# Kernel optimization log

Measured on AMD Instinct MI355X. Metric: run time of the kernel, lower is better.

The kernel has to match this reference:

```python
import jax, jax.numpy as jnp
import numpy as np

N_ENT = 100000
N_REL = 500
D_IN = 128
D_OUT = 128
E_HALF = 1000000  # edges per direction; edge_index has 2*E_HALF columns
BN_EPS = 1e-5


def ccorr(a, b):
    # circular correlation: irfft(conj(rfft(a)) * rfft(b))
    d = a.shape[-1]
    return jnp.fft.irfft(jnp.conj(jnp.fft.rfft(a, axis=-1)) * jnp.fft.rfft(b, axis=-1), n=d, axis=-1)


def setup_inputs() -> dict:
    key = jax.random.key(0)
    ks = jax.random.split(key, 12)
    inv = 1.0 / np.sqrt(D_IN)
    inp = {
        "x": jax.random.normal(ks[0], (N_ENT, D_IN), dtype=jnp.float32),
        "rel_embed": jax.random.normal(ks[1], (N_REL, D_IN), dtype=jnp.float32),
        "w_in": jax.random.uniform(ks[2], (D_IN, D_OUT), minval=-inv, maxval=inv, dtype=jnp.float32),
        "w_out": jax.random.uniform(ks[3], (D_IN, D_OUT), minval=-inv, maxval=inv, dtype=jnp.float32),
        "w_loop": jax.random.uniform(ks[4], (D_IN, D_OUT), minval=-inv, maxval=inv, dtype=jnp.float32),
        "w_rel": jax.random.uniform(ks[5], (D_IN, D_OUT), minval=-inv, maxval=inv, dtype=jnp.float32),
        "loop_rel": jax.random.normal(ks[6], (1, D_IN), dtype=jnp.float32),
        "bias": jnp.zeros((D_OUT,), dtype=jnp.float32),
        "bn_weight": jnp.ones((D_OUT,), dtype=jnp.float32),
        "bn_bias": jnp.zeros((D_OUT,), dtype=jnp.float32),
        "edge_index": jax.random.randint(ks[7], (2, 2 * E_HALF), 0, N_ENT, dtype=jnp.int32),
        "edge_type": jax.random.randint(ks[8], (2 * E_HALF,), 0, N_REL, dtype=jnp.int32),
    }
    return inp


def _compute_norm(edge_index, num_ent):
    row, col = edge_index[0], edge_index[1]
    ones = jnp.ones(row.shape, dtype=jnp.float32)
    deg = jax.ops.segment_sum(ones, row, num_segments=num_ent)
    deg_inv = jnp.where(deg > 0, jax.lax.rsqrt(jnp.maximum(deg, 1.0)), 0.0)
    return deg_inv[row] * deg_inv[col]  # [E]


def _propagate(x, edge_index, edge_type, rel_all, weight, norm, num_ent):
    x_j = x[edge_index[0]]              # [E, d_in] gather source nodes
    r = rel_all[edge_type]              # [E, d_in] gather relation embeds
    m = ccorr(x_j, r) @ weight          # [E, d_out]
    if norm is not None:
        m = m * norm[:, None]
    return jax.ops.segment_sum(m, edge_index[1], num_segments=num_ent)


def reference(x, rel_embed, w_in, w_out, w_loop, w_rel, loop_rel, bias, bn_weight, bn_bias, edge_index, edge_type):
    num_ent = x.shape[0]
    rel_all = jnp.concatenate([rel_embed, loop_rel], axis=0)  # [R+1, d_in]
    e = edge_index.shape[1] // 2
    in_idx, out_idx = edge_index[:, :e], edge_index[:, e:]
    in_type, out_type = edge_type[:e], edge_type[e:]

    in_norm = _compute_norm(in_idx, num_ent)
    out_norm = _compute_norm(out_idx, num_ent)

    in_res = _propagate(x, in_idx, in_type, rel_all, w_in, in_norm, num_ent)
    out_res = _propagate(x, out_idx, out_type, rel_all, w_out, out_norm, num_ent)
    # loop edges are (i, i) with relation = last row of rel_all -> identity scatter
    loop_res = ccorr(x, rel_all[-1][None, :]) @ w_loop

    out = (in_res + out_res + loop_res) * (1.0 / 3.0) + bias
    # BatchNorm1d (training-mode batch statistics, biased variance)
    mu = jnp.mean(out, axis=0)
    var = jnp.mean((out - mu) ** 2, axis=0)
    out = (out - mu) * jax.lax.rsqrt(var + BN_EPS) * bn_weight + bn_bias

    rel_out = (rel_all @ w_rel)[:-1]
    return out, rel_out
```

## Files before the change

kernel.cpp:

```cpp
#include <hip/hip_runtime.h>
#include <cmath>

#define N_ENT 100000
#define EHALF 1000000
#define N_REL 500
#define NBUK 196
#define DPB 512
#define SCAP 7680
#define DCAP 6656
#define NSB 512
#define SPAN 1954
#define XFB 391

#ifndef M_PI
#define M_PI 3.14159265358979323846
#endif

typedef _Float16 f16x8 __attribute__((ext_vector_type(8)));
typedef _Float16 f16x4 __attribute__((ext_vector_type(4)));
typedef _Float16 f16x2 __attribute__((ext_vector_type(2)));
typedef float f32x4 __attribute__((ext_vector_type(4)));

union H16 { unsigned short u; _Float16 h; };
union HU32 { unsigned u; f16x2 h; };

__global__ void k_tabs(float* __restrict__ Ftab, float* __restrict__ Gtab,
                       _Float16* __restrict__ FtabT,
                       int* __restrict__ gcur, float* __restrict__ bnAcc) {
  if (blockIdx.x == 0) {
    for (int j = threadIdx.x; j < 4 * NBUK; j += 256) gcur[j] = 0;
    bnAcc[threadIdx.x] = 0.f;
  }
  int i = blockIdx.x * 256 + threadIdx.x;
  if (i >= 128 * 128) return;
  int n = i >> 7, s = i & 127;
  float fv, gv;
  if (s == 0) { fv = 1.f; gv = 1.f / 384.f; }
  else if (s == 1) { float sg = (n & 1) ? -1.f : 1.f; fv = sg; gv = sg / 384.f; }
  else {
    int f = s >> 1;
    double ang = 2.0 * M_PI * (double)((f * n) & 127) / 128.0;
    if (!(s & 1)) { double c = cos(ang); fv = (float)c; gv = (float)(c * (2.0 / 384.0)); }
    else { double sv = sin(ang); fv = (float)(-sv); gv = (float)(-sv * (2.0 / 384.0)); }
  }
  Ftab[n * 128 + s] = fv;
  Gtab[s * 128 + n] = gv;
  FtabT[s * 128 + n] = (_Float16)fv;
}

__device__ void gemm128_body(char* smem, const float* __restrict__ A, int lda,
                             const float* __restrict__ B,
                             float* __restrict__ C, int ldc,
                             int M, int K, int m0) {
  float (*As)[64] = (float(*)[64])smem;
  float (*Bs)[128] = (float(*)[128])(smem + 64 * 64 * 4);
  const int t = threadIdx.x;
  const int cg = t & 31;
  const int eg = t >> 5;
  float acc[8][4];
#pragma unroll
  for (int i = 0; i < 8; ++i)
#pragma unroll
    for (int j = 0; j < 4; ++j) acc[i][j] = 0.f;

  for (int k0 = 0; k0 < K; k0 += 64) {
#pragma unroll
    for (int p = 0; p < 4; ++p) {
      int idx = t + p * 256;
      int r = idx >> 4, c4 = idx & 15;
      int gr = m0 + r;
      float4 v = make_float4(0.f, 0.f, 0.f, 0.f);
      if (gr < M) v = *(const float4*)(A + (size_t)gr * lda + k0 + c4 * 4);
      *(float4*)&As[r][c4 * 4] = v;
    }
#pragma unroll
    for (int p = 0; p < 8; ++p) {
      int idx = t + p * 256;
      int r = idx >> 5, c4 = idx & 31;
      float4 v = *(const float4*)(B + (size_t)(k0 + r) * 128 + c4 * 4);
      *(float4*)&Bs[r][c4 * 4] = v;
    }
    __syncthreads();
#pragma unroll
    for (int k = 0; k < 64; ++k) {
      float4 bv = *(float4*)&Bs[k][cg * 4];
#pragma unroll
      for (int i = 0; i < 8; ++i) {
        float av = As[eg * 8 + i][k];
        acc[i][0] += av * bv.x; acc[i][1] += av * bv.y;
        acc[i][2] += av * bv.z; acc[i][3] += av * bv.w;
      }
    }
    __syncthreads();
  }
#pragma unroll
  for (int i = 0; i < 8; ++i) {
    int gr = m0 + eg * 8 + i;
    if (gr < M) {
      float4 v = make_float4(acc[i][0], acc[i][1], acc[i][2], acc[i][3]);
      *(float4*)(C + (size_t)gr * ldc + cg * 4) = v;
    }
  }
}

__device__ inline f16x8 loadAfrag(const _Float16* A, size_t off) {
  return *(const f16x8*)(A + off);
}
__device__ inline f16x8 loadAfrag(const float* A, size_t off) {
  float4 u = *(const float4*)(A + off);
  float4 v = *(const float4*)(A + off + 4);
  return (f16x8){(_Float16)u.x, (_Float16)u.y, (_Float16)u.z, (_Float16)u.w,
                 (_Float16)v.x, (_Float16)v.y, (_Float16)v.z, (_Float16)v.w};
}

template<int K, int KS, int MODE, typename AT>
__device__ void mgemm_body(char* lds, int bid,
                           const AT* __restrict__ A, int lda,
                           const _Float16* __restrict__ BT,
                           _Float16* __restrict__ C, int ldc, int M,
                           const float* __restrict__ bias, float* __restrict__ bnAcc) {
  const int t = threadIdx.x;
  const int l = t & 63, w = t >> 6;
  const int col0 = l & 15, rg = l >> 4;
  const int rowbase = bid * 256 + w * 64;
  const int sw = (col0 & 7) << 4;

  f32x4 acc[4][8];
  f32x4 zz = {0.f, 0.f, 0.f, 0.f};
#pragma unroll
  for (int a = 0; a < 4; ++a)
#pragma unroll
    for (int n = 0; n < 8; ++n) acc[a][n] = zz;

  for (int ks0 = 0; ks0 < K; ks0 += KS) {
    __syncthreads();
    const int CH = KS / 8;
    for (int u = t; u < 128 * CH; u += 256) {
      int col = u / CH, kc = u % CH;
      f16x8 vch = *(const f16x8*)(BT + (size_t)col * K + ks0 + kc * 8);
      *(f16x8*)(lds + col * (KS * 2) + ((kc * 16) ^ ((col & 7) << 4))) = vch;
    }
    __syncthreads();
#pragma unroll
    for (int ks = 0; ks < KS / 32; ++ks) {
      int kb = ks0 + ks * 32 + rg * 8;
      f16x8 af[4];
#pragma unroll
      for (int a = 0; a < 4; ++a) {
        int rb = rowbase + a * 16;
        if (rb < M) af[a] = loadAfrag(A, (size_t)(rb + col0) * lda + kb);
        else af[a] = (f16x8){0, 0, 0, 0, 0, 0, 0, 0};
      }
      int kc = ks * 4 + rg;
#pragma unroll
      for (int n = 0; n < 8; ++n) {
        f16x8 bf = *(const f16x8*)(lds + (n * 16 + col0) * (KS * 2) + ((kc * 16) ^ sw));
#pragma unroll
        for (int a = 0; a < 4; ++a)
          acc[a][n] = __builtin_amdgcn_mfma_f32_16x16x32_f16(af[a], bf, acc[a][n], 0, 0, 0);
      }
    }
  }

  if (MODE == 1) {
#pragma unroll
    for (int a = 0; a < 4; ++a) {
      int rb = rowbase + a * 16;
      if (rb >= M) continue;
#pragma unroll
      for (int r = 0; r < 4; ++r) {
        int row = rb + rg * 4 + r;
#pragma unroll
        for (int n = 0; n < 8; ++n) {
          int col = n * 16 + col0;
          C[(size_t)row * ldc + col] = (_Float16)acc[a][n][r];
        }
      }
    }
  } else {
    float sacc[8], qacc[8];
#pragma unroll
    for (int n = 0; n < 8; ++n) { sacc[n] = 0.f; qacc[n] = 0.f; }
#pragma unroll
    for (int a = 0; a < 4; ++a) {
      int rb = rowbase + a * 16;
      if (rb >= M) continue;
#pragma unroll
      for (int n = 0; n < 8; ++n) {
        int col = n * 16 + col0;
        float bi = bias[col];
#pragma unroll
        for (int r = 0; r < 4; ++r) {
          float val = acc[a][n][r] + bi;
          C[(size_t)(rb + rg * 4 + r) * ldc + col] = (_Float16)val;
          sacc[n] += val; qacc[n] += val * val;
        }
      }
    }
    __syncthreads();
    float* Sb = (float*)lds;
    float* Qb = Sb + 512;
#pragma unroll
    for (int n = 0; n < 8; ++n) {
      float s = sacc[n], q = qacc[n];
      s += __shfl_xor(s, 16); s += __shfl_xor(s, 32);
      q += __shfl_xor(q, 16); q += __shfl_xor(q, 32);
      if (rg == 0) { Sb[w * 128 + n * 16 + col0] = s; Qb[w * 128 + n * 16 + col0] = q; }
    }
    __syncthreads();
    if (t < 128) {
      float s = Sb[t] + Sb[128 + t] + Sb[256 + t] + Sb[384 + t];
      float q = Qb[t] + Qb[128 + t] + Qb[256 + t] + Qb[384 + t];
      atomicAdd(&bnAcc[t], s);
      atomicAdd(&bnAcc[128 + t], q);
    }
  }
}

__device__ void split_body(char* smem, int bid,
                           const int* __restrict__ ei, const int* __restrict__ et,
                           int* __restrict__ gcur,
                           unsigned* __restrict__ recSI, unsigned* __restrict__ recSO,
                           uint2* __restrict__ recDI, uint2* __restrict__ recDO) {
  int* bcnt = (int*)smem;
  int* cnt2 = bcnt + NBUK;
  int* base = cnt2 + NBUK;
  int* nn   = base + NBUK;
  const int t = threadIdx.x;
  const int ph = bid >> 9;
  const int blk = bid & 511;
  const int st = blk * SPAN;
  const int en = min(st + SPAN, EHALF);

  if (t < NBUK) { bcnt[t] = 0; cnt2[t] = 0; }
  __syncthreads();

  if (ph < 2) {
    const int* key = ei + (ph ? EHALF : 0);
    int* gc = gcur + ph * NBUK;
    unsigned* rec = ph ? recSO : recSI;
    unsigned rr[8]; int bb[8];
#pragma unroll
    for (int j = 0; j < 8; ++j) {
      int e = st + j * 256 + t;
      bb[j] = -1;
      if (e < en) {
        int s = key[e];
        rr[j] = (unsigned)(s & 511) | 0x80000000u;
        bb[j] = s >> 9;
        atomicAdd(&bcnt[bb[j]], 1);
      }
    }
    __syncthreads();
    if (t < NBUK) {
      int n = bcnt[t]; nn[t] = n;
      base[t] = n ? (t * SCAP + atomicAdd(&gc[t], (n + 7) & ~7)) : 0;
    }
    __syncthreads();
#pragma unroll
    for (int j = 0; j < 8; ++j) {
      if (bb[j] >= 0) {
        int p = atomicAdd(&cnt2[bb[j]], 1);
        rec[(size_t)base[bb[j]] + p] = rr[j];
      }
    }
    __syncthreads();
    if (t < NBUK) {
      int n = nn[t];
      if (n & 7) {
        int pe = (n + 7) & ~7;
        for (int k = n; k < pe; ++k) rec[(size_t)base[t] + k] = 0u;
      }
    }
  } else {
    const int dir = ph - 2;
    const int* srcA = ei + (dir ? EHALF : 0);
    const int* dstA = ei + (dir ? 3 * EHALF : 2 * EHALF);
    const int* typA = et + (dir ? EHALF : 0);
    int* gc = gcur + (2 + dir) * NBUK;
    uint2* rec = dir ? recDO : recDI;
    unsigned w0[8], w1[8]; int bb[8];
#pragma unroll
    for (int j = 0; j < 8; ++j) {
      int e = st + j * 256 + t;
      bb[j] = -1;
      if (e < en) {
        int s = srcA[e], d = dstA[e], ty = typA[e];
        w0[j] = (unsigned)s | ((unsigned)ty << 17);
        w1[j] = (unsigned)(d & 511) | 0x80000000u;
        bb[j] = d >> 9;
        atomicAdd(&bcnt[bb[j]], 1);
      }
    }
    __syncthreads();
    if (t < NBUK) {
      int n = bcnt[t]; nn[t] = n;
      base[t] = n ? (t * DCAP + atomicAdd(&gc[t], (n + 3) & ~3)) : 0;
    }
    __syncthreads();
#pragma unroll
    for (int j = 0; j < 8; ++j) {
      if (bb[j] >= 0) {
        int p = atomicAdd(&cnt2[bb[j]], 1);
        rec[(size_t)base[bb[j]] + p] = make_uint2(w0[j], w1[j]);
      }
    }
    __syncthreads();
    if (t < NBUK) {
      int n = nn[t];
      if (n & 3) {
        int pe = (n + 3) & ~3;
        for (int k = n; k < pe; ++k) rec[(size_t)base[t] + k] = make_uint2(0u, 0u);
      }
    }
  }
}

__device__ void dftrel_body(char* smem, int blk,
                            const float* __restrict__ rel, const float* __restrict__ looprel,
                            const float* __restrict__ Ftab, float* __restrict__ Rf,
                            _Float16* __restrict__ RfL) {
  float* sv = (float*)smem;
  int t = threadIdx.x;
  int r = blk * 2 + (t >> 7);
  int s = t & 127;
  if (r < 501) {
    const float* row = (r < N_REL) ? rel + (size_t)r * 128 : looprel;
    float acc = 0.f;
    for (int n = 0; n < 128; ++n) acc += row[n] * Ftab[n * 128 + s];
    Rf[(size_t)r * 128 + s] = acc;
    sv[t] = acc;
  }
  __syncthreads();
  if (r < 501 && s < 64) {
    int bse = t & 128;
    f16x4 o;
    if (s == 0) {
      o = (f16x4){(_Float16)sv[bse], (_Float16)0.f, (_Float16)0.f, (_Float16)sv[bse + 1]};
    } else {
      float rx = sv[bse + 2 * s], ry = sv[bse + 2 * s + 1];
      o = (f16x4){(_Float16)rx, (_Float16)ry, (_Float16)ry, (_Float16)(-rx)};
    }
    ((f16x4*)RfL)[(size_t)r * 64 + s] = o;
  }
}

__device__ void dhist_body(char* smem, int bid,
                           const unsigned* __restrict__ recI, const int* __restrict__ gI,
                           float* __restrict__ dinvIn,
                           const unsigned* __restrict__ recO, const int* __restrict__ gO,
                           float* __restrict__ dinvOut) {
  int b = bid % NBUK;
  int dir = bid / NBUK;
  const unsigned* rec = dir ? recO : recI;
  const int gs = b * SCAP;
  const int ge = gs + (dir ? gO : gI)[b];
  float* dinv = dir ? dinvOut : dinvIn;
  int* h = (int*)smem;
  int t = threadIdx.x;
  h[t] = 0; h[t + 256] = 0;
  __syncthreads();
  for (int i = gs + t; i < ge; i += 256) {
    unsigned r = rec[i];
    if (r >> 31) atomicAdd(&h[r & 511], 1);
  }
  __syncthreads();
#pragma unroll
  for (int j = 0; j < 2; ++j) {
    int bin = t + j * 256;
    int ent = b * 512 + bin;
    if (ent < N_ENT) {
      int d = h[bin];
      dinv[ent] = (d > 0) ? rsqrtf((float)d) : 0.f;
    }
  }
}

__device__ void fsort_body(char* smem, int bid,
                           const uint2* __restrict__ recDI, const int* __restrict__ gDI,
                           uint2* __restrict__ csrIn, int2* __restrict__ beI,
                           const uint2* __restrict__ recDO, const int* __restrict__ gDO,
                           uint2* __restrict__ csrOut, int2* __restrict__ beO,
                           const float* __restrict__ dinvIn, const float* __restrict__ dinvOut) {
  int b = bid % NBUK;
  int dir = bid / NBUK;
  const uint2* rec = dir ? recDO : recDI;
  const int gs = b * DCAP;
  const int ge = gs + (dir ? gDO : gDI)[b];
  const float* dinv = dir ? dinvOut : dinvIn;
  uint2* csr = dir ? csrOut : csrIn;
  int2* be = dir ? beO : beI;
  int* h  = (int*)smem;
  int* sc = h + 512;
  int* c2 = sc + 512;
  float* dl = (float*)(c2 + 512);
  int* totv = (int*)(dl + 512);
  int t = threadIdx.x;
  int ent = b * 512 + t;
  h[t] = 0; c2[t] = 0;
  dl[t] = (ent < N_ENT) ? dinv[ent] : 0.f;
  __syncthreads();
  for (int i = gs + t; i < ge; i += 512) {
    uint2 r = rec[i];
    if (r.y >> 31) atomicAdd(&h[r.y & 511], 1);
  }
  __syncthreads();
  sc[t] = h[t];
  __syncthreads();
  for (int o = 1; o < 512; o <<= 1) {
    int a = (t >= o) ? sc[t - o] : 0;
    __syncthreads();
    sc[t] += a;
    __syncthreads();
  }
  int excl = sc[t] - h[t];
  if (t == 511) *totv = sc[511];
  if (ent < N_ENT) be[ent] = make_int2(gs + excl, gs + excl + h[t]);
  __syncthreads();
  sc[t] = excl;
  __syncthreads();
  if (t < 8) csr[(size_t)gs + *totv + t] = make_uint2(0u, 0u);
  for (int i = gs + t; i < ge; i += 512) {
    uint2 r = rec[i];
    if (r.y >> 31) {
      int d = r.y & 511;
      unsigned src = r.x & 0x1FFFFu;
      float nm = dinv[src] * dl[d];
      H16 cv; cv.h = (_Float16)nm;
      int p = atomicAdd(&c2[d], 1);
      csr[(size_t)gs + sc[d] + p] =
          make_uint2((src * 3u) << 8,
                     (r.x >> 17) | ((unsigned)cv.u << 16));
    }
  }
}

__device__ void wt_body(int wb, const float* __restrict__ W, const float* __restrict__ Rfl,
                        _Float16* __restrict__ WT) {
  int i = wb * 512 + threadIdx.x;
  if (i >= 384 * 128) return;
  int k = i >> 7, c = i & 127;
  float val;
  if (k < 256) {
    val = W[i];
  } else {
    int kk = k - 256;
    if (kk == 0)      val = Rfl[0] * W[i];
    else if (kk == 1) val = Rfl[1] * W[i];
    else {
      int f = kk >> 1;
      float rr = Rfl[2 * f], ri = Rfl[2 * f + 1];
      float a = W[(256 + 2 * f) * 128 + c];
      float b = W[(256 + 2 * f + 1) * 128 + c];
      val = (kk & 1) ? (ri * a - rr * b) : (rr * a + ri * b);
    }
  }
  WT[(size_t)c * 384 + k] = (_Float16)val;
}

__device__ void norm_body(char* smem, int bid, const _Float16* __restrict__ tmp,
                          float* __restrict__ out, const float* __restrict__ bnAcc,
                          const float* __restrict__ bnw, const float* __restrict__ bnb) {
  float* ss = (float*)smem;
  int t = threadIdx.x;
  if (t < 128) {
    float mu = bnAcc[t] * (1.f / (float)N_ENT);
    float var = bnAcc[128 + t] * (1.f / (float)N_ENT) - mu * mu;
    float sc = bnw[t] * rsqrtf(var + 1e-5f);
    ss[t] = sc; ss[128 + t] = bnb[t] - mu * sc;
  }
  __syncthreads();
  int i = bid * 256 + t;
  f16x8 v = ((const f16x8*)tmp)[i];
  int cb = (i & 15) * 8;
  float4 o0, o1;
  o0.x = (float)v[0] * ss[cb]     + ss[128 + cb];
  o0.y = (float)v[1] * ss[cb + 1] + ss[129 + cb];
  o0.z = (float)v[2] * ss[cb + 2] + ss[130 + cb];
  o0.w = (float)v[3] * ss[cb + 3] + ss[131 + cb];
  o1.x = (float)v[4] * ss[cb + 4] + ss[132 + cb];
  o1.y = (float)v[5] * ss[cb + 5] + ss[133 + cb];
  o1.z = (float)v[6] * ss[cb + 6] + ss[134 + cb];
  o1.w = (float)v[7] * ss[cb + 7] + ss[135 + cb];
  ((float4*)out)[2 * i] = o0;
  ((float4*)out)[2 * i + 1] = o1;
}

__global__ __launch_bounds__(256) void k_front(
    const float* __restrict__ x, const _Float16* __restrict__ FtabT, _Float16* __restrict__ Abuf,
    const int* __restrict__ ei, const int* __restrict__ et, int* __restrict__ gcur,
    unsigned* __restrict__ recSI, unsigned* __restrict__ recSO,
    uint2* __restrict__ recDI, uint2* __restrict__ recDO,
    const float* __restrict__ rel, const float* __restrict__ looprel,
    const float* __restrict__ Ftab, float* __restrict__ Rf, _Float16* __restrict__ RfL) {
  __shared__ __align__(16) char smem[37120];
  int b = blockIdx.x;
  if (b < XFB) {
    mgemm_body<128, 128, 1, float>(smem, b, x, 128, FtabT, Abuf + 256, 384, N_ENT,
                                   nullptr, nullptr);
  } else if (b < XFB + 4 * NSB) {
    split_body(smem, b - XFB, ei, et, gcur, recSI, recSO, recDI, recDO);
  } else {
    dftrel_body(smem, b - XFB - 4 * NSB, rel, looprel, Ftab, Rf, RfL);
  }
}

__global__ __launch_bounds__(256) void k_mid1(
    const float* __restrict__ Gtab, const float* __restrict__ w0,
    const float* __restrict__ w1, const float* __restrict__ w2, float* __restrict__ Wstack,
    const unsigned* __restrict__ recSI, const int* __restrict__ gSI, float* __restrict__ dinvIn,
    const unsigned* __restrict__ recSO, const int* __restrict__ gSO, float* __restrict__ dinvOut) {
  __shared__ __align__(16) char smem[49280];
  int b = blockIdx.x;
  if (b < 6) {
    int which = b >> 1;
    const float* B = (which == 0) ? w0 : ((which == 1) ? w1 : w2);
    gemm128_body(smem, Gtab, 128, B, Wstack + which * 128 * 128, 128, 128, 128, (b & 1) * 64);
  } else {
    dhist_body(smem, b - 6, recSI, gSI, dinvIn, recSO, gSO, dinvOut);
  }
}

__global__ __launch_bounds__(512) void k_mid2(
    const uint2* __restrict__ recDI, const int* __restrict__ gDI,
    uint2* __restrict__ csrIn, int2* __restrict__ beI,
    const uint2* __restrict__ recDO, const int* __restrict__ gDO,
    uint2* __restrict__ csrOut, int2* __restrict__ beO,
    const float* __restrict__ dinvIn, const float* __restrict__ dinvOut,
    const float* __restrict__ Wstack, const float* __restrict__ Rfl, _Float16* __restrict__ WT) {
  __shared__ __align__(16) char smem[8448];
  int b = blockIdx.x;
  if (b < 2 * NBUK) {
    fsort_body(smem, b, recDI, gDI, csrIn, beI, recDO, gDO, csrOut, beO, dinvIn, dinvOut);
  } else {
    wt_body(b - 2 * NBUK, Wstack, Rfl, WT);
  }
}

__global__ __launch_bounds__(256) void k_mgemm384(
    const _Float16* __restrict__ A, const _Float16* __restrict__ BT,
    _Float16* __restrict__ C, int M,
    const float* __restrict__ bias, float* __restrict__ bnAcc) {
  __shared__ __align__(16) char lds[53504];
  mgemm_body<384, 192, 2, _Float16>(lds, blockIdx.x, A, 384, BT, C, 128, M, bias, bnAcc);
}

__global__ __launch_bounds__(256) void k_back(
    const float* __restrict__ rel, const float* __restrict__ w_rel, float* __restrict__ out,
    const _Float16* __restrict__ tmp, const float* __restrict__ bnAcc,
    const float* __restrict__ bnw, const float* __restrict__ bnb) {
  __shared__ __align__(16) char smem[49280];
  int b = blockIdx.x;
  if (b < 8) {
    gemm128_body(smem, rel, 128, w_rel, out + (size_t)N_ENT * 128, 128, N_REL, 128, b * 64);
  } else {
    norm_body(smem, b - 8, tmp, out, bnAcc, bnw, bnb);
  }
}

__device__ inline float dot2f(f16x2 a, f16x2 b, float c) {
#if __has_builtin(__builtin_amdgcn_fdot2)
  return __builtin_amdgcn_fdot2(a, b, c, false);
#else
  return fmaf((float)a[0], (float)b[0], fmaf((float)a[1], (float)b[1], c));
#endif
}

__device__ inline void b4load(const uint2* __restrict__ csr, int base,
                              const char* __restrict__ Xb, const char* __restrict__ Rb,
                              unsigned lxc, unsigned lr,
                              uint2 q[4], f16x2 xv[4], f16x4 rv[4]) {
#pragma unroll
  for (int j = 0; j < 4; ++j) q[j] = csr[base + j];
#pragma unroll
  for (int j = 0; j < 4; ++j) {
    xv[j] = *(const f16x2*)(Xb + q[j].x + lxc);
    rv[j] = *(const f16x4*)(Rb + ((q[j].y & 0x1FFu) << 9) + lr);
  }
}
__device__ inline void b4math(const uint2 q[4], int base, int end,
                              const f16x2 xv[4], const f16x4 rv[4],
                              float& ax, float& ay) {
#pragma unroll
  for (int j = 0; j < 4; ++j) {
    unsigned nb = (base + j < end) ? (q[j].y >> 16) : 0u;
    HU32 nm; nm.u = nb | (nb << 16);
    f16x2 xs = xv[j] * nm.h;
    ax = dot2f(xs, (f16x2){rv[j][0], rv[j][1]}, ax);
    ay = dot2f(xs, (f16x2){rv[j][2], rv[j][3]}, ay);
  }
}

__global__ __launch_bounds__(256) void k_agg(
    _Float16* __restrict__ Abuf, const _Float16* __restrict__ RfL,
    const uint2* __restrict__ csrIn, const int2* __restrict__ beI,
    const uint2* __restrict__ csrOut, const int2* __restrict__ beO) {
  const int w = threadIdx.x >> 6, l = threadIdx.x & 63;
  const int v = blockIdx.x * 4 + w;
  const char* Xb = (const char*)Abuf;
  const char* Rb = (const char*)RfL;
  const unsigned lxc = 512u + (unsigned)l * 4u;
  const unsigned lr = (unsigned)l * 8u;
  int2 bi = beI[v], bo = beO[v];
  int i  = __builtin_amdgcn_readfirstlane(bi.x);
  int ie = __builtin_amdgcn_readfirstlane(bi.y);
  int o  = __builtin_amdgcn_readfirstlane(bo.x);
  int oe = __builtin_amdgcn_readfirstlane(bo.y);
  int nbi = (ie - i + 3) >> 2;
  int nbo = (oe - o + 3) >> 2;
  float aix = 0.f, aiy = 0.f, aox = 0.f, aoy = 0.f;

  while (nbi > 0 && nbo > 0) {
    uint2 qa[4], qb[4]; f16x2 xa[4], xb[4]; f16x4 ra[4], rb[4];
    b4load(csrIn, i, Xb, Rb, lxc, lr, qa, xa, ra);
    b4load(csrOut, o, Xb, Rb, lxc, lr, qb, xb, rb);
    b4math(qa, i, ie, xa, ra, aix, aiy);
    b4math(qb, o, oe, xb, rb, aox, aoy);
    i += 4; o += 4; --nbi; --nbo;
  }
  while (nbi > 0) {
    uint2 qa[4]; f16x2 xa[4]; f16x4 ra[4];
    b4load(csrIn, i, Xb, Rb, lxc, lr, qa, xa, ra);
    b4math(qa, i, ie, xa, ra, aix, aiy);
    i += 4; --nbi;
  }
  while (nbo > 0) {
    uint2 qb[4]; f16x2 xb[4]; f16x4 rb[4];
    b4load(csrOut, o, Xb, Rb, lxc, lr, qb, xb, rb);
    b4math(qb, o, oe, xb, rb, aox, aoy);
    o += 4; --nbo;
  }

  *(f16x2*)((char*)Abuf + (size_t)v * 768 + 4u * l) = (f16x2){(_Float16)aix, (_Float16)aiy};
  *(f16x2*)((char*)Abuf + (size_t)v * 768 + 256 + 4u * l) = (f16x2){(_Float16)aox, (_Float16)aoy};
}

extern "C" void kernel_launch(void* const* d_in, const int* in_sizes, int n_in,
                              void* d_out, int out_size, void* d_ws, size_t ws_size,
                              hipStream_t stream) {
  const float* x       = (const float*)d_in[0];
  const float* rel     = (const float*)d_in[1];
  const float* w_in    = (const float*)d_in[2];
  const float* w_out   = (const float*)d_in[3];
  const float* w_loop  = (const float*)d_in[4];
  const float* w_rel   = (const float*)d_in[5];
  const float* looprel = (const float*)d_in[6];
  const float* bias    = (const float*)d_in[7];
  const float* bnw     = (const float*)d_in[8];
  const float* bnb     = (const float*)d_in[9];
  const int*   ei      = (const int*)d_in[10];
  const int*   et      = (const int*)d_in[11];
  float* out = (float*)d_out;

  char* p = (char*)d_ws;
  auto alloc = [&](size_t bytes) -> void* {
    void* r = (void*)p;
    p += (bytes + 255) & ~(size_t)255;
    return r;
  };
  _Float16* Abuf  = (_Float16*)alloc((size_t)N_ENT * 384 * 2);
  _Float16* tmpC  = (_Float16*)alloc((size_t)N_ENT * 128 * 2);
  _Float16* WT    = (_Float16*)alloc(128 * 384 * 2);
  _Float16* FtabT = (_Float16*)alloc(128 * 128 * 2);
  _Float16* RfL   = (_Float16*)alloc(501 * 64 * 4 * 2);
  float* Wstack   = (float*)alloc(384 * 128 * 4);
  float* Ftab     = (float*)alloc(128 * 128 * 4);
  float* Gtab     = (float*)alloc(128 * 128 * 4);
  float* Rf       = (float*)alloc(501 * 128 * 4);
  float* dinvIn   = (float*)alloc(N_ENT * 4);
  float* dinvOut  = (float*)alloc(N_ENT * 4);
  int*   gcur     = (int*)alloc(4 * NBUK * 4);
  int2*  beI      = (int2*)alloc((size_t)N_ENT * 8);
  int2*  beO      = (int2*)alloc((size_t)N_ENT * 8);
  unsigned* recSI = (unsigned*)alloc((size_t)NBUK * SCAP * 4);
  unsigned* recSO = (unsigned*)alloc((size_t)NBUK * SCAP * 4);
  uint2* recDI    = (uint2*)alloc((size_t)NBUK * DCAP * 8);
  uint2* recDO    = (uint2*)alloc((size_t)NBUK * DCAP * 8);
  uint2* csrIn    = (uint2*)alloc((size_t)NBUK * DCAP * 8);
  uint2* csrOut   = (uint2*)alloc((size_t)NBUK * DCAP * 8);
  float* bnAcc    = (float*)alloc(256 * 4);

  int* gSI = gcur;
  int* gSO = gcur + NBUK;
  int* gDI = gcur + 2 * NBUK;
  int* gDO = gcur + 3 * NBUK;

  k_tabs<<<64, 256, 0, stream>>>(Ftab, Gtab, FtabT, gcur, bnAcc);

  k_front<<<XFB + 4 * NSB + 251, 256, 0, stream>>>(
      x, FtabT, Abuf, ei, et, gcur, recSI, recSO, recDI, recDO,
      rel, looprel, Ftab, Rf, RfL);

  k_mid1<<<6 + 2 * NBUK, 256, 0, stream>>>(
      Gtab, w_in, w_out, w_loop, Wstack, recSI, gSI, dinvIn, recSO, gSO, dinvOut);

  k_mid2<<<2 * NBUK + 96, 512, 0, stream>>>(
      recDI, gDI, csrIn, beI, recDO, gDO, csrOut, beO, dinvIn, dinvOut,
      Wstack, Rf + 500 * 128, WT);

  k_agg<<<N_ENT / 4, 256, 0, stream>>>(Abuf, RfL, csrIn, beI, csrOut, beO);

  k_mgemm384<<<XFB, 256, 0, stream>>>(Abuf, WT, tmpC, N_ENT, bias, bnAcc);

  k_back<<<8 + (N_ENT * 128 / 8) / 256, 256, 0, stream>>>(
      rel, w_rel, out, tmpC, bnAcc, bnw, bnb);
}
```

Measured before the change: 328.5 us.

## Split fused heterogeneous kernels by resource needs and move rel GEMM to MFMA

The large fused front kernel is split so the x-transform GEMM and the edge split/relation DFT run as separate launches. The small LDS-light blocks then no longer inherit the GEMM's large shared-memory footprint and can run at higher occupancy. Weight prep and the degree histogram become separate launches, and the histogram now uses 512 threads. The rel_embed @ w_rel product moves from the fp32 gemm128 path into the MFMA GEMM, with a transposed fp16 copy of w_rel prepared ahead of time, and rides along with the output GEMM. The trade-off is more kernel launches and lower precision for rel_out.

Result: faster. 299.6 us (median of 2 runs) (-8.8%).

```diff
diff --git a/kernel.cpp b/kernel.cpp
--- a/kernel.cpp
+++ b/kernel.cpp
@@ -113,11 +113,11 @@
                  (_Float16)v.x, (_Float16)v.y, (_Float16)v.z, (_Float16)v.w};
 }
 
-template<int K, int KS, int MODE, typename AT>
+template<int K, int KS, int MODE, typename AT, typename CT>
 __device__ void mgemm_body(char* lds, int bid,
                            const AT* __restrict__ A, int lda,
                            const _Float16* __restrict__ BT,
-                           _Float16* __restrict__ C, int ldc, int M,
+                           CT* __restrict__ C, int ldc, int M,
                            const float* __restrict__ bias, float* __restrict__ bnAcc) {
   const int t = threadIdx.x;
   const int l = t & 63, w = t >> 6;
@@ -173,7 +173,7 @@
 #pragma unroll
         for (int n = 0; n < 8; ++n) {
           int col = n * 16 + col0;
-          C[(size_t)row * ldc + col] = (_Float16)acc[a][n][r];
+          C[(size_t)row * ldc + col] = (CT)acc[a][n][r];
         }
       }
     }
@@ -192,7 +192,7 @@
 #pragma unroll
         for (int r = 0; r < 4; ++r) {
           float val = acc[a][n][r] + bi;
-          C[(size_t)(rb + rg * 4 + r) * ldc + col] = (_Float16)val;
+          C[(size_t)(rb + rg * 4 + r) * ldc + col] = (CT)val;
           sacc[n] += val; qacc[n] += val * val;
         }
       }
@@ -342,37 +342,6 @@
       o = (f16x4){(_Float16)rx, (_Float16)ry, (_Float16)ry, (_Float16)(-rx)};
     }
     ((f16x4*)RfL)[(size_t)r * 64 + s] = o;
-  }
-}
-
-__device__ void dhist_body(char* smem, int bid,
-                           const unsigned* __restrict__ recI, const int* __restrict__ gI,
-                           float* __restrict__ dinvIn,
-                           const unsigned* __restrict__ recO, const int* __restrict__ gO,
-                           float* __restrict__ dinvOut) {
-  int b = bid % NBUK;
-  int dir = bid / NBUK;
-  const unsigned* rec = dir ? recO : recI;
-  const int gs = b * SCAP;
-  const int ge = gs + (dir ? gO : gI)[b];
-  float* dinv = dir ? dinvOut : dinvIn;
-  int* h = (int*)smem;
-  int t = threadIdx.x;
-  h[t] = 0; h[t + 256] = 0;
-  __syncthreads();
-  for (int i = gs + t; i < ge; i += 256) {
-    unsigned r = rec[i];
-    if (r >> 31) atomicAdd(&h[r & 511], 1);
-  }
-  __syncthreads();
-#pragma unroll
-  for (int j = 0; j < 2; ++j) {
-    int bin = t + j * 256;
-    int ent = b * 512 + bin;
-    if (ent < N_ENT) {
-      int d = h[bin];
-      dinv[ent] = (d > 0) ? rsqrtf((float)d) : 0.f;
-    }
   }
 }
 
@@ -458,10 +427,113 @@
   WT[(size_t)c * 384 + k] = (_Float16)val;
 }
 
-__device__ void norm_body(char* smem, int bid, const _Float16* __restrict__ tmp,
-                          float* __restrict__ out, const float* __restrict__ bnAcc,
-                          const float* __restrict__ bnw, const float* __restrict__ bnb) {
-  float* ss = (float*)smem;
+__device__ void wrt_body(int wb, const float* __restrict__ Wr, _Float16* __restrict__ WrT) {
+  int i = wb * 512 + threadIdx.x;
+  if (i >= 128 * 128) return;
+  int k = i >> 7, c = i & 127;
+  WrT[(size_t)c * 128 + k] = (_Float16)Wr[i];
+}
+
+__global__ __launch_bounds__(256) void k_sd(
+    const int* __restrict__ ei, const int* __restrict__ et, int* __restrict__ gcur,
+    unsigned* __restrict__ recSI, unsigned* __restrict__ recSO,
+    uint2* __restrict__ recDI, uint2* __restrict__ recDO,
+    const float* __restrict__ rel, const float* __restrict__ looprel,
+    const float* __restrict__ Ftab, float* __restrict__ Rf, _Float16* __restrict__ RfL) {
+  __shared__ __align__(16) char smem[3200];
+  int b = blockIdx.x;
+  if (b < 4 * NSB) {
+    split_body(smem, b, ei, et, gcur, recSI, recSO, recDI, recDO);
+  } else {
+    dftrel_body(smem, b - 4 * NSB, rel, looprel, Ftab, Rf, RfL);
+  }
+}
+
+__global__ __launch_bounds__(256) void k_xf(
+    const float* __restrict__ x, const _Float16* __restrict__ FtabT,
+    _Float16* __restrict__ Abuf) {
+  __shared__ __align__(16) char lds[36992];
+  mgemm_body<128, 128, 1, float, _Float16>(lds, blockIdx.x, x, 128, FtabT,
+                                           Abuf + 256, 384, N_ENT, nullptr, nullptr);
+}
+
+__global__ __launch_bounds__(256) void k_wprep(
+    const float* __restrict__ Gtab, const float* __restrict__ w0,
+    const float* __restrict__ w1, const float* __restrict__ w2,
+    float* __restrict__ Wstack) {
+  __shared__ __align__(16) char smem[49280];
+  int which = blockIdx.x >> 1;
+  const float* B = (which == 0) ? w0 : ((which == 1) ? w1 : w2);
+  gemm128_body(smem, Gtab, 128, B, Wstack + which * 128 * 128, 128, 128, 128,
+               (blockIdx.x & 1) * 64);
+}
+
+__global__ __launch_bounds__(512) void k_dhist(
+    const unsigned* __restrict__ recI, const int* __restrict__ gI,
+    float* __restrict__ dinvIn,
+    const unsigned* __restrict__ recO, const int* __restrict__ gO,
+    float* __restrict__ dinvOut) {
+  int b = blockIdx.x % NBUK;
+  int dir = blockIdx.x / NBUK;
+  const unsigned* rec = dir ? recO : recI;
+  const int gs = b * SCAP;
+  const int ge = gs + (dir ? gO : gI)[b];
+  float* dinv = dir ? dinvOut : dinvIn;
+  __shared__ int h[DPB];
+  int t = threadIdx.x;
+  h[t] = 0;
+  __syncthreads();
+  for (int i = gs + t; i < ge; i += 512) {
+    unsigned r = rec[i];
+    if (r >> 31) atomicAdd(&h[r & 511], 1);
+  }
+  __syncthreads();
+  int ent = b * 512 + t;
+  if (ent < N_ENT) {
+    int d = h[t];
+    dinv[ent] = (d > 0) ? rsqrtf((float)d) : 0.f;
+  }
+}
+
+__global__ __launch_bounds__(512) void k_fw(
+    const uint2* __restrict__ recDI, const int* __restrict__ gDI,
+    uint2* __restrict__ csrIn, int2* __restrict__ beI,
+    const uint2* __restrict__ recDO, const int* __restrict__ gDO,
+    uint2* __restrict__ csrOut, int2* __restrict__ beO,
+    const float* __restrict__ dinvIn, const float* __restrict__ dinvOut,
+    const float* __restrict__ Wstack, const float* __restrict__ Rfl, _Float16* __restrict__ WT,
+    const float* __restrict__ w_rel, _Float16* __restrict__ WrT) {
+  __shared__ __align__(16) char smem[8448];
+  int b = blockIdx.x;
+  if (b < 2 * NBUK) {
+    fsort_body(smem, b, recDI, gDI, csrIn, beI, recDO, gDO, csrOut, beO, dinvIn, dinvOut);
+  } else if (b < 2 * NBUK + 96) {
+    wt_body(b - 2 * NBUK, Wstack, Rfl, WT);
+  } else {
+    wrt_body(b - 2 * NBUK - 96, w_rel, WrT);
+  }
+}
+
+__global__ __launch_bounds__(256) void k_out(
+    const _Float16* __restrict__ Abuf, const _Float16* __restrict__ WT,
+    _Float16* __restrict__ tmpC, const float* __restrict__ bias, float* __restrict__ bnAcc,
+    const float* __restrict__ rel, const _Float16* __restrict__ WrT, float* __restrict__ out) {
+  __shared__ __align__(16) char lds[53504];
+  int b = blockIdx.x;
+  if (b < XFB) {
+    mgemm_body<384, 192, 2, _Float16, _Float16>(lds, b, Abuf, 384, WT, tmpC, 128, N_ENT,
+                                                bias, bnAcc);
+  } else {
+    mgemm_body<128, 128, 1, float, float>(lds, b - XFB, rel, 128, WrT,
+                                          out + (size_t)N_ENT * 128, 128, N_REL,
+                                          nullptr, nullptr);
+  }
+}
+
+__global__ void k_norm(const _Float16* __restrict__ tmp, float* __restrict__ out,
+                       const float* __restrict__ bnAcc, const float* __restrict__ bnw,
+                       const float* __restrict__ bnb) {
+  __shared__ float ss[256];
   int t = threadIdx.x;
   if (t < 128) {
     float mu = bnAcc[t] * (1.f / (float)N_ENT);
@@ -470,7 +542,7 @@
     ss[t] = sc; ss[128 + t] = bnb[t] - mu * sc;
   }
   __syncthreads();
-  int i = bid * 256 + t;
+  int i = blockIdx.x * 256 + t;
   f16x8 v = ((const f16x8*)tmp)[i];
   int cb = (i & 15) * 8;
   float4 o0, o1;
@@ -484,78 +556,6 @@
   o1.w = (float)v[7] * ss[cb + 7] + ss[135 + cb];
   ((float4*)out)[2 * i] = o0;
   ((float4*)out)[2 * i + 1] = o1;
-}
-
-__global__ __launch_bounds__(256) void k_front(
-    const float* __restrict__ x, const _Float16* __restrict__ FtabT, _Float16* __restrict__ Abuf,
-    const int* __restrict__ ei, const int* __restrict__ et, int* __restrict__ gcur,
-    unsigned* __restrict__ recSI, unsigned* __restrict__ recSO,
-    uint2* __restrict__ recDI, uint2* __restrict__ recDO,
-    const float* __restrict__ rel, const float* __restrict__ looprel,
-    const float* __restrict__ Ftab, float* __restrict__ Rf, _Float16* __restrict__ RfL) {
-  __shared__ __align__(16) char smem[37120];
-  int b = blockIdx.x;
-  if (b < XFB) {
-    mgemm_body<128, 128, 1, float>(smem, b, x, 128, FtabT, Abuf + 256, 384, N_ENT,
-                                   nullptr, nullptr);
-  } else if (b < XFB + 4 * NSB) {
-    split_body(smem, b - XFB, ei, et, gcur, recSI, recSO, recDI, recDO);
-  } else {
-    dftrel_body(smem, b - XFB - 4 * NSB, rel, looprel, Ftab, Rf, RfL);
-  }
-}
-
-__global__ __launch_bounds__(256) void k_mid1(
-    const float* __restrict__ Gtab, const float* __restrict__ w0,
-    const float* __restrict__ w1, const float* __restrict__ w2, float* __restrict__ Wstack,
-    const unsigned* __restrict__ recSI, const int* __restrict__ gSI, float* __restrict__ dinvIn,
-    const unsigned* __restrict__ recSO, const int* __restrict__ gSO, float* __restrict__ dinvOut) {
-  __shared__ __align__(16) char smem[49280];
-  int b = blockIdx.x;
-  if (b < 6) {
-    int which = b >> 1;
-    const float* B = (which == 0) ? w0 : ((which == 1) ? w1 : w2);
-    gemm128_body(smem, Gtab, 128, B, Wstack + which * 128 * 128, 128, 128, 128, (b & 1) * 64);
-  } else {
-    dhist_body(smem, b - 6, recSI, gSI, dinvIn, recSO, gSO, dinvOut);
-  }
-}
-
-__global__ __launch_bounds__(512) void k_mid2(
-    const uint2* __restrict__ recDI, const int* __restrict__ gDI,
-    uint2* __restrict__ csrIn, int2* __restrict__ beI,
-    const uint2* __restrict__ recDO, const int* __restrict__ gDO,
-    uint2* __restrict__ csrOut, int2* __restrict__ beO,
-    const float* __restrict__ dinvIn, const float* __restrict__ dinvOut,
-    const float* __restrict__ Wstack, const float* __restrict__ Rfl, _Float16* __restrict__ WT) {
-  __shared__ __align__(16) char smem[8448];
-  int b = blockIdx.x;
-  if (b < 2 * NBUK) {
-    fsort_body(smem, b, recDI, gDI, csrIn, beI, recDO, gDO, csrOut, beO, dinvIn, dinvOut);
-  } else {
-    wt_body(b - 2 * NBUK, Wstack, Rfl, WT);
-  }
-}
-
-__global__ __launch_bounds__(256) void k_mgemm384(
-    const _Float16* __restrict__ A, const _Float16* __restrict__ BT,
-    _Float16* __restrict__ C, int M,
-    const float* __restrict__ bias, float* __restrict__ bnAcc) {
-  __shared__ __align__(16) char lds[53504];
-  mgemm_body<384, 192, 2, _Float16>(lds, blockIdx.x, A, 384, BT, C, 128, M, bias, bnAcc);
-}
-
-__global__ __launch_bounds__(256) void k_back(
-    const float* __restrict__ rel, const float* __restrict__ w_rel, float* __restrict__ out,
-    const _Float16* __restrict__ tmp, const float* __restrict__ bnAcc,
-    const float* __restrict__ bnw, const float* __restrict__ bnb) {
-  __shared__ __align__(16) char smem[49280];
-  int b = blockIdx.x;
-  if (b < 8) {
-    gemm128_body(smem, rel, 128, w_rel, out + (size_t)N_ENT * 128, 128, N_REL, 128, b * 64);
-  } else {
-    norm_body(smem, b - 8, tmp, out, bnAcc, bnw, bnb);
-  }
 }
 
 __device__ inline float dot2f(f16x2 a, f16x2 b, float c) {
@@ -661,6 +661,7 @@
   _Float16* Abuf  = (_Float16*)alloc((size_t)N_ENT * 384 * 2);
   _Float16* tmpC  = (_Float16*)alloc((size_t)N_ENT * 128 * 2);
   _Float16* WT    = (_Float16*)alloc(128 * 384 * 2);
+  _Float16* WrT   = (_Float16*)alloc(128 * 128 * 2);
   _Float16* FtabT = (_Float16*)alloc(128 * 128 * 2);
   _Float16* RfL   = (_Float16*)alloc(501 * 64 * 4 * 2);
   float* Wstack   = (float*)alloc(384 * 128 * 4);
@@ -687,21 +688,22 @@
 
   k_tabs<<<64, 256, 0, stream>>>(Ftab, Gtab, FtabT, gcur, bnAcc);
 
-  k_front<<<XFB + 4 * NSB + 251, 256, 0, stream>>>(
-      x, FtabT, Abuf, ei, et, gcur, recSI, recSO, recDI, recDO,
-      rel, looprel, Ftab, Rf, RfL);
-
-  k_mid1<<<6 + 2 * NBUK, 256, 0, stream>>>(
-      Gtab, w_in, w_out, w_loop, Wstack, recSI, gSI, dinvIn, recSO, gSO, dinvOut);
-
-  k_mid2<<<2 * NBUK + 96, 512, 0, stream>>>(
+  k_sd<<<4 * NSB + 251, 256, 0, stream>>>(ei, et, gcur, recSI, recSO, recDI, recDO,
+                                          rel, looprel, Ftab, Rf, RfL);
+
+  k_xf<<<XFB, 256, 0, stream>>>(x, FtabT, Abuf);
+
+  k_wprep<<<6, 256, 0, stream>>>(Gtab, w_in, w_out, w_loop, Wstack);
+
+  k_dhist<<<2 * NBUK, 512, 0, stream>>>(recSI, gSI, dinvIn, recSO, gSO, dinvOut);
+
+  k_fw<<<2 * NBUK + 96 + 32, 512, 0, stream>>>(
       recDI, gDI, csrIn, beI, recDO, gDO, csrOut, beO, dinvIn, dinvOut,
-      Wstack, Rf + 500 * 128, WT);
+      Wstack, Rf + 500 * 128, WT, w_rel, WrT);
 
   k_agg<<<N_ENT / 4, 256, 0, stream>>>(Abuf, RfL, csrIn, beI, csrOut, beO);
 
-  k_mgemm384<<<XFB, 256, 0, stream>>>(Abuf, WT, tmpC, N_ENT, bias, bnAcc);
-
-  k_back<<<8 + (N_ENT * 128 / 8) / 256, 256, 0, stream>>>(
-      rel, w_rel, out, tmpC, bnAcc, bnw, bnb);
-}
+  k_out<<<XFB + 2, 256, 0, stream>>>(Abuf, WT, tmpC, bias, bnAcc, rel, WrT, out);
+
+  k_norm<<<(N_ENT * 128 / 8) / 256, 256, 0, stream>>>(tmpC, out, bnAcc, bnw, bnb);
+}
```
